# Kernel tuning notes

Measured on AMD Instinct MI355X. Metric: run time of the kernel, lower is better.

Reference implementation:

```python
import jax, jax.numpy as jnp
import numpy as np
import math

S, B, H, NH, HD = 2048, 1, 4096, 32, 128
ROT = HD // 2  # 2D RoPE: each half of head_dim gets its own rotary embedding


def _rotate_half(x):
    x1, x2 = jnp.split(x, 2, axis=-1)
    return jnp.concatenate((-x2, x1), axis=-1)


def _rope_tables(max_pos, dim):
    inv_freq = 1.0 / (10000.0 ** (jnp.arange(0, dim, 2, dtype=jnp.float32) / dim))
    freqs = jnp.arange(max_pos, dtype=jnp.float32)[:, None] * inv_freq[None, :]  # [P, dim/2]
    emb = jnp.concatenate((freqs, freqs), axis=-1)  # [P, dim]
    return jnp.cos(emb), jnp.sin(emb)


def _apply_rope(q, k, cos_t, sin_t, pid):
    # q,k: [S,B,NH,ROT]; pid: [S,B]
    c = cos_t[pid][:, :, None, :]  # [S,B,1,ROT]
    s = sin_t[pid][:, :, None, :]
    return q * c + _rotate_half(q) * s, k * c + _rotate_half(k) * s


def setup_inputs() -> dict:
    key = jax.random.key(0)
    k1, k2, k3, k4, k5 = jax.random.split(key, 5)
    hidden_states = jax.random.normal(k1, (S, B, H), dtype=jnp.float32)
    pos = jnp.arange(S, dtype=jnp.int32)[None, :]          # [1,S] standard positions
    blk = jnp.zeros((1, S), dtype=jnp.int32)                # block positions (pre-gmask all zeros)
    position_ids = jnp.stack([pos, blk], axis=1)            # [B,2,S]
    # causal mask: True = masked out
    attention_mask = jnp.triu(jnp.ones((S, S), dtype=bool), k=1)[None, None]  # [B,1,S,S]
    Wqkv = jax.random.normal(k2, (3 * H, H), dtype=jnp.float32) * 0.02
    bqkv = jax.random.normal(k3, (3 * H,), dtype=jnp.float32) * 0.02
    Wd = jax.random.normal(k4, (H, H), dtype=jnp.float32) * 0.02
    bd = jax.random.normal(k5, (H,), dtype=jnp.float32) * 0.02
    return {"hidden_states": hidden_states, "position_ids": position_ids,
            "attention_mask": attention_mask, "layer_id": 5,
            "Wqkv": Wqkv, "bqkv": bqkv, "Wd": Wd, "bd": bd}


def reference(hidden_states, position_ids, attention_mask, layer_id, Wqkv, bqkv, Wd, bd):
    # QKV projection: [S,B,H] -> [S,B,NH,3*HD]
    mixed = hidden_states @ Wqkv.T + bqkv
    mixed = mixed.reshape(S, B, NH, 3 * HD)
    q, k, v = jnp.split(mixed, 3, axis=-1)  # each [S,B,NH,HD]

    # 2D rotary position embedding on the two head-dim halves
    q1, q2 = jnp.split(q, 2, axis=-1)
    k1, k2 = jnp.split(k, 2, axis=-1)
    cos_t, sin_t = _rope_tables(S, ROT)
    pid = position_ids[:, 0, :].T   # [S,B]
    bid = position_ids[:, 1, :].T   # [S,B]
    q1, k1 = _apply_rope(q1, k1, cos_t, sin_t, pid)
    q2, k2 = _apply_rope(q2, k2, cos_t, sin_t, bid)
    q = jnp.concatenate([q1, q2], axis=-1)
    k = jnp.concatenate([k1, k2], axis=-1)

    # layer-scaled attention scores
    coeff = float(layer_id + 1)
    q = q / (math.sqrt(HD) * coeff)
    scores = jnp.einsum('sbnd,tbnd->bnst', q, k)  # [B,NH,S,S]
    scores = jnp.where(attention_mask, jnp.float32(-10000.0), scores)
    scores = scores.astype(jnp.float32) * coeff
    probs = jax.nn.softmax(scores, axis=-1).astype(hidden_states.dtype)

    ctx = jnp.einsum('bnst,tbnd->sbnd', probs, v).reshape(S, B, NH * HD)
    return ctx @ Wd.T + bd  # [S,B,H]
```

## Files before the change

kernel.cpp:

```cpp
#include <hip/hip_runtime.h>


#define S_LEN 2048
#define NHEAD 32
#define HDIM 128
#define HID 4096

typedef float f32x4 __attribute__((ext_vector_type(4)));
typedef __bf16 bf16x8 __attribute__((ext_vector_type(8)));
typedef __bf16 bf16x4 __attribute__((ext_vector_type(4)));
typedef _Float16 f16x4 __attribute__((ext_vector_type(4)));
typedef _Float16 f16x8 __attribute__((ext_vector_type(8)));

__device__ __forceinline__ void gload16(const void* g, void* l) {
  __builtin_amdgcn_global_load_lds(
      (const __attribute__((address_space(1))) void*)g,
      (__attribute__((address_space(3))) void*)l, 16, 0, 0);
}

__global__ __launch_bounds__(256) void cvt_f32_bf16_kernel(
    const float* __restrict__ in, __bf16* __restrict__ out, int n4) {
  int i = blockIdx.x * 256 + threadIdx.x;
  if (i >= n4) return;
  f32x4 v = *(const f32x4*)(in + (size_t)i * 4);
  bf16x4 o;
  o[0] = (__bf16)v[0]; o[1] = (__bf16)v[1];
  o[2] = (__bf16)v[2]; o[3] = (__bf16)v[3];
  *(bf16x4*)(out + (size_t)i * 4) = o;
}

__device__ __forceinline__ void stage_half(const __bf16* __restrict__ G,
                                           int grow0, int Kstride, int kofs,
                                           __bf16* lds_half, int tid) {
#pragma unroll
  for (int i = 0; i < 2; ++i) {
    int idx = i * 512 + tid;
    int rr = idx >> 3;
    int offp = (idx & 7) * 16;
    int off = offp ^ ((rr & 7) << 4);
    const char* src =
        (const char*)(G + (size_t)(grow0 + rr) * Kstride + kofs) + off;
    char* dst = (char*)lds_half + idx * 16;
    gload16(src, dst);
  }
}

__device__ __forceinline__ bf16x8 ldsfrag(const __bf16* hb, int rowin, int ks,
                                          int lg) {
  int off = ((ks * 64 + lg * 16) ^ ((rowin & 7) << 4));
  return *(const bf16x8*)((const char*)hb + rowin * 128 + off);
}

#define READ_A(DST, SLOT)                                                     \
  _Pragma("unroll") for (int mi = 0; mi < 4; ++mi)                            \
      _Pragma("unroll") for (int ks = 0; ks < 2; ++ks) DST[mi][ks] =          \
      ldsfrag(SLOT, wm * 64 + mi * 16 + lr, ks, lg);

#define READ_B(DST, SLOT)                                                     \
  _Pragma("unroll") for (int nj = 0; nj < 2; ++nj)                            \
      _Pragma("unroll") for (int ks = 0; ks < 2; ++ks) DST[nj][ks] =          \
      ldsfrag(SLOT, wn * 32 + nj * 16 + lr, ks, lg);

#define MFMA_Q(MH, NH, AFR, BFR)                                              \
  __builtin_amdgcn_s_setprio(1);                                              \
  _Pragma("unroll") for (int mi = 0; mi < 4; ++mi)                            \
      _Pragma("unroll") for (int nj = 0; nj < 2; ++nj)                        \
          _Pragma("unroll") for (int ks = 0; ks < 2; ++ks)                    \
              acc[MH][NH][mi][nj] =                                           \
      __builtin_amdgcn_mfma_f32_16x16x32_bf16(AFR[mi][ks], BFR[nj][ks],       \
                                              acc[MH][NH][mi][nj], 0, 0, 0);  \
  __builtin_amdgcn_s_setprio(0);

#define BAR asm volatile("s_barrier" ::: "memory");

template <int OUT_MODE>
__global__ __launch_bounds__(512, 2) void gemm256_kernel(
    const __bf16* __restrict__ A, const __bf16* __restrict__ B,
    const float* __restrict__ bias, void* __restrict__ Cout, int M, int N,
    int Kstride, int klen, int mtiles, int ksplit) {
  __shared__ __align__(16) __bf16 As[2][2][128 * 64];
  __shared__ __align__(16) __bf16 Bs[2][2][128 * 64];
  const int tid = threadIdx.x;
  int bid = blockIdx.x;
  int kh = 0;
  if (ksplit == 2) { kh = bid & 1; bid >>= 1; }
  const int kbase = kh * klen;
  int per_patch = mtiles * 8;
  int p = bid / per_patch, r = bid % per_patch;
  int mt = r % mtiles, nt = p * 8 + r / mtiles;
  int m0 = mt * 256, n0 = nt * 256;
  const int wid = tid >> 6, l = tid & 63;
  const int wm = wid >> 2, wn = wid & 3;
  const int lr = l & 15, lg = l >> 4;
  const int nk = klen >> 6;

  f32x4 acc[2][2][4][2];
#pragma unroll
  for (int a = 0; a < 2; ++a)
#pragma unroll
    for (int b = 0; b < 2; ++b)
#pragma unroll
      for (int c = 0; c < 4; ++c)
#pragma unroll
        for (int d = 0; d < 2; ++d) acc[a][b][c][d] = 0.f;

  stage_half(A, m0, Kstride, kbase, &As[0][0][0], tid);
  stage_half(B, n0, Kstride, kbase, &Bs[0][0][0], tid);
  stage_half(B, n0 + 128, Kstride, kbase, &Bs[0][1][0], tid);
  stage_half(A, m0 + 128, Kstride, kbase, &As[0][1][0], tid);
  if (nk > 1) {
    stage_half(A, m0, Kstride, kbase + 64, &As[1][0][0], tid);
    stage_half(B, n0, Kstride, kbase + 64, &Bs[1][0][0], tid);
    stage_half(B, n0 + 128, Kstride, kbase + 64, &Bs[1][1][0], tid);
    asm volatile("s_waitcnt vmcnt(6)" ::: "memory");
  } else {
    asm volatile("s_waitcnt vmcnt(0)" ::: "memory");
  }
  BAR;

  for (int t = 0; t < nk; ++t) {
    const int cur = t & 1, nxt = cur ^ 1;
    const int kt1 = kbase + (t + 1) * 64;
    const int kt2 = kbase + (t + 2) * 64;
    const bool s1 = (t + 1 < nk), s2 = (t + 2 < nk);
    bf16x8 a[4][2], b0[2][2], b1[2][2];

    READ_A(a, &As[cur][0][0]);
    READ_B(b0, &Bs[cur][0][0]);
    if (s1) stage_half(A, m0 + 128, Kstride, kt1, &As[nxt][1][0], tid);
    BAR;
    MFMA_Q(0, 0, a, b0);

    READ_B(b1, &Bs[cur][1][0]);
    if (s2) stage_half(A, m0, Kstride, kt2, &As[cur][0][0], tid);
    BAR;
    MFMA_Q(0, 1, a, b1);

    READ_A(a, &As[cur][1][0]);
    if (s2) stage_half(B, n0 + 128, Kstride, kt2, &Bs[cur][1][0], tid);
    BAR;
    MFMA_Q(1, 1, a, b1);

    if (s2) stage_half(B, n0, Kstride, kt2, &Bs[cur][0][0], tid);
    BAR;
    MFMA_Q(1, 0, a, b0);
    if (s2)
      asm volatile("s_waitcnt vmcnt(6)" ::: "memory");
    else
      asm volatile("s_waitcnt vmcnt(0)" ::: "memory");
  }

  float* outF = (float*)Cout;
  if (OUT_MODE == 2) outF += (size_t)kh * M * N;
#pragma unroll
  for (int mh = 0; mh < 2; ++mh)
#pragma unroll
    for (int nh = 0; nh < 2; ++nh)
#pragma unroll
      for (int mi = 0; mi < 4; ++mi)
#pragma unroll
        for (int nj = 0; nj < 2; ++nj) {
          int row = m0 + mh * 128 + wm * 64 + mi * 16 + lg * 4;
          int col = n0 + nh * 128 + wn * 32 + nj * 16 + lr;
          float bv = (OUT_MODE == 2) ? 0.f : bias[col];
          f32x4 v = acc[mh][nh][mi][nj];
#pragma unroll
          for (int j = 0; j < 4; ++j) {
            float o = v[j] + bv;
            if (OUT_MODE == 1)
              ((__bf16*)Cout)[(size_t)(row + j) * N + col] = (__bf16)o;
            else
              outF[(size_t)(row + j) * N + col] = o;
          }
        }
}

__global__ __launch_bounds__(256) void reduce_addbias_kernel(
    const float* __restrict__ p0, const float* __restrict__ p1,
    const float* __restrict__ bias, float* __restrict__ out) {
  int i = blockIdx.x * 256 + threadIdx.x;
  int col = (i * 4) & (HID - 1);
  f32x4 a = *(const f32x4*)(p0 + (size_t)i * 4);
  f32x4 b = *(const f32x4*)(p1 + (size_t)i * 4);
  f32x4 c = *(const f32x4*)(bias + col);
  a = a + b + c;
  *(f32x4*)(out + (size_t)i * 4) = a;
}

__global__ __launch_bounds__(256) void rope_kernel(
    const __bf16* __restrict__ qkv, const int* __restrict__ pos_ids,
    __bf16* __restrict__ Q, __bf16* __restrict__ K, _Float16* __restrict__ VT) {
  int h = blockIdx.x & 31, sb = blockIdx.x >> 5;
  int s0 = sb * 64;
  int t = threadIdx.x;
  __shared__ float cs[64][2][2][32];
  __shared__ _Float16 vs[64][132];

  for (int idx = t; idx < 64 * 64; idx += 256) {
    int sl = idx >> 6, half = (idx >> 5) & 1, i = idx & 31;
    int p = pos_ids[half * S_LEN + s0 + sl];
    float f = powf(10000.f, -(float)i / 32.f);
    float ang = (float)p * f;
    cs[sl][half][0][i] = cosf(ang);
    cs[sl][half][1][i] = sinf(ang);
  }
#pragma unroll
  for (int c = 0; c < 4; c++) {
    int chunk = c * 256 + t;
    int slv = chunk >> 4, co = (chunk & 15) * 8;
    const __bf16* vsrc =
        qkv + (size_t)(s0 + slv) * (NHEAD * 3 * HDIM) + h * 384 + 256 + co;
    bf16x8 vv = *(const bf16x8*)vsrc;
    f16x4 a, b;
#pragma unroll
    for (int j = 0; j < 4; j++) {
      a[j] = (_Float16)(float)vv[j];
      b[j] = (_Float16)(float)vv[4 + j];
    }
    *(f16x4*)&vs[slv][co] = a;
    *(f16x4*)&vs[slv][co + 4] = b;
  }
  __syncthreads();

  {
    int sl = t >> 2, role = t & 3;
    int isK = role >> 1, half = role & 1;
    const __bf16* src = qkv + (size_t)(s0 + sl) * (NHEAD * 3 * HDIM) + h * 384 +
                        isK * 128 + half * 64;
    float scale = isK ? 1.f : 0.08838834764831845f;
    float x[64];
    bf16x8 buf[8];
#pragma unroll
    for (int c = 0; c < 8; c++) buf[c] = *(const bf16x8*)(src + c * 8);
#pragma unroll
    for (int c = 0; c < 8; c++)
#pragma unroll
      for (int j = 0; j < 8; j++) x[c * 8 + j] = (float)buf[c][j];
    bf16x8 ob[8];
#pragma unroll
    for (int i = 0; i < 64; i++) {
      int ii = i & 31;
      float cv = cs[sl][half][0][ii], sv = cs[sl][half][1][ii];
      float partner = (i < 32) ? x[i + 32] : x[i - 32];
      float sgn = (i < 32) ? -1.f : 1.f;
      float o = (x[i] * cv + sgn * partner * sv) * scale;
      ob[i >> 3][i & 7] = (__bf16)o;
    }
    __bf16* dst = (isK ? K : Q) + ((size_t)h * S_LEN + s0 + sl) * HDIM + half * 64;
#pragma unroll
    for (int c = 0; c < 8; c++) *(bf16x8*)(dst + c * 8) = ob[c];
  }

#pragma unroll
  for (int c = 0; c < 4; c++) {
    int chunk = c * 256 + t;
    int d = chunk >> 3, so = (chunk & 7) * 8;
    f16x8 o;
#pragma unroll
    for (int j = 0; j < 8; j++) o[j] = vs[so + j][d];
    *(f16x8*)(VT + ((size_t)h * HDIM + d) * S_LEN + s0 + so) = o;
  }
}

__global__ __launch_bounds__(256, 2) void attn_kernel(
    const __bf16* __restrict__ Q, const __bf16* __restrict__ K,
    const _Float16* __restrict__ VT, __bf16* __restrict__ ctx) {
  int b = blockIdx.x;
  int h = b & 31;
  int x = b >> 5;
  int qb = (b < 256) ? (15 - x) : (x - 8);
  int w = threadIdx.x >> 6, l = threadIdx.x & 63;
  int lr = l & 15, lg = l >> 4;
  int q0 = qb * 128 + w * 32;
  const __bf16* Qh = Q + (size_t)h * S_LEN * HDIM;
  const __bf16* Kh = K + (size_t)h * S_LEN * HDIM;
  const _Float16* Vh = VT + (size_t)h * HDIM * S_LEN;

  bf16x8 qfA[4], qfB[4];
#pragma unroll
  for (int kk = 0; kk < 4; kk++) {
    qfA[kk] = *(const bf16x8*)(Qh + (size_t)(q0 + lr) * HDIM + kk * 32 + lg * 8);
    qfB[kk] =
        *(const bf16x8*)(Qh + (size_t)(q0 + 16 + lr) * HDIM + kk * 32 + lg * 8);
  }

  f32x4 accA[8], accB[8];
#pragma unroll
  for (int tt = 0; tt < 8; tt++) { accA[tt] = 0.f; accB[tt] = 0.f; }
  float mA = -INFINITY, lsA = 0.f, mB = -INFINITY, lsB = 0.f;
  int qgA = q0 + lr, qgB = q0 + 16 + lr;
  int qmax = q0 + 31;

  for (int kv0 = 0; kv0 <= qmax; kv0 += 32) {
    f32x4 stA0 = 0.f, stA1 = 0.f, stB0 = 0.f, stB1 = 0.f;
#pragma unroll
    for (int kk = 0; kk < 4; kk++) {
      bf16x8 kf0 =
          *(const bf16x8*)(Kh + (size_t)(kv0 + lr) * HDIM + kk * 32 + lg * 8);
      bf16x8 kf1 = *(const bf16x8*)(Kh + (size_t)(kv0 + 16 + lr) * HDIM +
                                    kk * 32 + lg * 8);
      stA0 = __builtin_amdgcn_mfma_f32_16x16x32_bf16(kf0, qfA[kk], stA0, 0, 0, 0);
      stB0 = __builtin_amdgcn_mfma_f32_16x16x32_bf16(kf0, qfB[kk], stB0, 0, 0, 0);
      stA1 = __builtin_amdgcn_mfma_f32_16x16x32_bf16(kf1, qfA[kk], stA1, 0, 0, 0);
      stB1 = __builtin_amdgcn_mfma_f32_16x16x32_bf16(kf1, qfB[kk], stB1, 0, 0, 0);
    }

    f16x4 vb0[8], vb1[8];
#pragma unroll
    for (int tt = 0; tt < 8; tt++) {
      const _Float16* vcol = Vh + (size_t)(tt * 16 + lr) * S_LEN;
      vb0[tt] = *(const f16x4*)(vcol + kv0 + lg * 4);
      vb1[tt] = *(const f16x4*)(vcol + kv0 + 16 + lg * 4);
    }

    float tmA = -INFINITY, tmB = -INFINITY;
#pragma unroll
    for (int j = 0; j < 4; j++) {
      int kvg0 = kv0 + lg * 4 + j;
      int kvg1 = kvg0 + 16;
      if (kvg0 > qgA) stA0[j] = -INFINITY;
      if (kvg1 > qgA) stA1[j] = -INFINITY;
      if (kvg0 > qgB) stB0[j] = -INFINITY;
      if (kvg1 > qgB) stB1[j] = -INFINITY;
      tmA = fmaxf(tmA, fmaxf(stA0[j], stA1[j]));
      tmB = fmaxf(tmB, fmaxf(stB0[j], stB1[j]));
    }
    tmA = fmaxf(tmA, __shfl_xor(tmA, 16));
    tmA = fmaxf(tmA, __shfl_xor(tmA, 32));
    tmB = fmaxf(tmB, __shfl_xor(tmB, 16));
    tmB = fmaxf(tmB, __shfl_xor(tmB, 32));
    int need = __any((tmA > mA) || (tmB > mB));
    float mnA = fmaxf(mA, tmA), mnB = fmaxf(mB, tmB);

    f16x4 paA0, paA1, paB0, paB1;
    float tsA = 0.f, tsB = 0.f;
#pragma unroll
    for (int j = 0; j < 4; j++) {
      float pA0 = __expf(stA0[j] - mnA);
      float pA1 = __expf(stA1[j] - mnA);
      float pB0 = __expf(stB0[j] - mnB);
      float pB1 = __expf(stB1[j] - mnB);
      tsA += pA0 + pA1;
      tsB += pB0 + pB1;
      paA0[j] = (_Float16)pA0; paA1[j] = (_Float16)pA1;
      paB0[j] = (_Float16)pB0; paB1[j] = (_Float16)pB1;
    }
    tsA += __shfl_xor(tsA, 16);
    tsA += __shfl_xor(tsA, 32);
    tsB += __shfl_xor(tsB, 16);
    tsB += __shfl_xor(tsB, 32);

    if (need) {
      float scA = __expf(mA - mnA), scB = __expf(mB - mnB);
      lsA = lsA * scA + tsA;
      lsB = lsB * scB + tsB;
      float sAj[4], sBj[4];
#pragma unroll
      for (int j = 0; j < 4; j++) {
        sAj[j] = __shfl(scA, lg * 4 + j);
        sBj[j] = __shfl(scB, lg * 4 + j);
      }
#pragma unroll
      for (int tt = 0; tt < 8; tt++)
#pragma unroll
        for (int j = 0; j < 4; j++) {
          accA[tt][j] *= sAj[j];
          accB[tt][j] *= sBj[j];
        }
    } else {
      lsA += tsA;
      lsB += tsB;
    }
    mA = mnA; mB = mnB;

#pragma unroll
    for (int tt = 0; tt < 8; tt++) {
      accA[tt] =
          __builtin_amdgcn_mfma_f32_16x16x16f16(paA0, vb0[tt], accA[tt], 0, 0, 0);
      accB[tt] =
          __builtin_amdgcn_mfma_f32_16x16x16f16(paB0, vb0[tt], accB[tt], 0, 0, 0);
      accA[tt] =
          __builtin_amdgcn_mfma_f32_16x16x16f16(paA1, vb1[tt], accA[tt], 0, 0, 0);
      accB[tt] =
          __builtin_amdgcn_mfma_f32_16x16x16f16(paB1, vb1[tt], accB[tt], 0, 0, 0);
    }
  }

  float rA[4], rB[4];
#pragma unroll
  for (int j = 0; j < 4; j++) {
    rA[j] = 1.f / __shfl(lsA, lg * 4 + j);
    rB[j] = 1.f / __shfl(lsB, lg * 4 + j);
  }
#pragma unroll
  for (int tt = 0; tt < 8; tt++) {
#pragma unroll
    for (int j = 0; j < 4; j++) {
      int qoA = q0 + lg * 4 + j;
      int qoB = q0 + 16 + lg * 4 + j;
      ctx[(size_t)qoA * (NHEAD * HDIM) + h * HDIM + tt * 16 + lr] =
          (__bf16)(accA[tt][j] * rA[j]);
      ctx[(size_t)qoB * (NHEAD * HDIM) + h * HDIM + tt * 16 + lr] =
          (__bf16)(accB[tt][j] * rB[j]);
    }
  }
}

extern "C" void kernel_launch(void* const* d_in, const int* in_sizes, int n_in,
                              void* d_out, int out_size, void* d_ws,
                              size_t ws_size, hipStream_t stream) {
  const float* hs = (const float*)d_in[0];
  const int* pos_ids = (const int*)d_in[1];
  const float* Wqkv = (const float*)d_in[4];
  const float* bqkv = (const float*)d_in[5];
  const float* Wd = (const float*)d_in[6];
  const float* bd = (const float*)d_in[7];
  float* out = (float*)d_out;

  char* ws = (char*)d_ws;
  constexpr size_t OFF_W = 16777216ULL;
  constexpr size_t OFF_QKV = OFF_W + 100663296ULL;
  constexpr size_t OFF_Q = OFF_QKV + 50331648ULL;
  constexpr size_t OFF_K = OFF_Q + 16777216ULL;
  constexpr size_t OFF_V = OFF_K + 16777216ULL;
  __bf16* hsb = (__bf16*)(ws);
  __bf16* wqkvb = (__bf16*)(ws + OFF_W);
  __bf16* wdb = (__bf16*)(ws + OFF_W);
  float* pk = (float*)(ws + OFF_W + 33554432ULL);
  __bf16* qkvb = (__bf16*)(ws + OFF_QKV);
  __bf16* ctxb = qkvb;
  __bf16* Qb = (__bf16*)(ws + OFF_Q);
  __bf16* Kb = (__bf16*)(ws + OFF_K);
  _Float16* Vtb = (_Float16*)(ws + OFF_V);

  cvt_f32_bf16_kernel<<<(S_LEN * HID) / 4 / 256, 256, 0, stream>>>(
      hs, hsb, S_LEN * HID / 4);
  cvt_f32_bf16_kernel<<<(3 * HID * HID) / 4 / 256, 256, 0, stream>>>(
      Wqkv, wqkvb, 3 * HID * HID / 4);

  gemm256_kernel<1><<<8 * 48, 512, 0, stream>>>(hsb, wqkvb, bqkv, qkvb, S_LEN,
                                                3 * HID, HID, HID, 8, 1);

  cvt_f32_bf16_kernel<<<(HID * HID) / 4 / 256, 256, 0, stream>>>(
      Wd, wdb, HID * HID / 4);

  rope_kernel<<<NHEAD * (S_LEN / 64), 256, 0, stream>>>(qkvb, pos_ids, Qb, Kb,
                                                        Vtb);

  attn_kernel<<<NHEAD * (S_LEN / 128), 256, 0, stream>>>(Qb, Kb, Vtb, ctxb);

  gemm256_kernel<2><<<2 * 8 * 16, 512, 0, stream>>>(ctxb, wdb, bd, pk, S_LEN,
                                                    HID, HID, HID / 2, 8, 2);
  reduce_addbias_kernel<<<(S_LEN * HID) / 4 / 256, 256, 0, stream>>>(
      pk, pk + (size_t)S_LEN * HID, bd, out);
}
```

Before: 565.7 us.

## Switch GEMMs to 128x256 tiles and drop split-K reduction for output projection

Replaces the 256x256-tile GEMM with a 128x256-tile kernel in which each wave computes a 64x64 sub-tile and the pipeline runs two k-substeps per 64-wide stage. The QKV projection now launches twice as many blocks, and the output projection drops split-K plus the separate reduce/bias kernel, writing fp32 output with bias directly. The aim is better CU occupancy and wave balance, and removing the partial-sum round trip through memory. In exchange each block has lower arithmetic intensity per loaded byte, and the output GEMM has only 256 blocks.

```diff
diff --git a/kernel.cpp b/kernel.cpp
--- a/kernel.cpp
+++ b/kernel.cpp
@@ -51,140 +51,110 @@
   return *(const bf16x8*)((const char*)hb + rowin * 128 + off);
 }
 
-#define READ_A(DST, SLOT)                                                     \
-  _Pragma("unroll") for (int mi = 0; mi < 4; ++mi)                            \
-      _Pragma("unroll") for (int ks = 0; ks < 2; ++ks) DST[mi][ks] =          \
-      ldsfrag(SLOT, wm * 64 + mi * 16 + lr, ks, lg);
-
-#define READ_B(DST, SLOT)                                                     \
-  _Pragma("unroll") for (int nj = 0; nj < 2; ++nj)                            \
-      _Pragma("unroll") for (int ks = 0; ks < 2; ++ks) DST[nj][ks] =          \
-      ldsfrag(SLOT, wn * 32 + nj * 16 + lr, ks, lg);
-
-#define MFMA_Q(MH, NH, AFR, BFR)                                              \
-  __builtin_amdgcn_s_setprio(1);                                              \
-  _Pragma("unroll") for (int mi = 0; mi < 4; ++mi)                            \
-      _Pragma("unroll") for (int nj = 0; nj < 2; ++nj)                        \
-          _Pragma("unroll") for (int ks = 0; ks < 2; ++ks)                    \
-              acc[MH][NH][mi][nj] =                                           \
-      __builtin_amdgcn_mfma_f32_16x16x32_bf16(AFR[mi][ks], BFR[nj][ks],       \
-                                              acc[MH][NH][mi][nj], 0, 0, 0);  \
-  __builtin_amdgcn_s_setprio(0);
-
 #define BAR asm volatile("s_barrier" ::: "memory");
 
-template <int OUT_MODE>
-__global__ __launch_bounds__(512, 2) void gemm256_kernel(
+template <int OUT_BF16>
+__global__ __launch_bounds__(512, 2) void gemm128_kernel(
     const __bf16* __restrict__ A, const __bf16* __restrict__ B,
     const float* __restrict__ bias, void* __restrict__ Cout, int M, int N,
-    int Kstride, int klen, int mtiles, int ksplit) {
-  __shared__ __align__(16) __bf16 As[2][2][128 * 64];
+    int K, int mtiles) {
+  __shared__ __align__(16) __bf16 As[2][128 * 64];
   __shared__ __align__(16) __bf16 Bs[2][2][128 * 64];
   const int tid = threadIdx.x;
   int bid = blockIdx.x;
-  int kh = 0;
-  if (ksplit == 2) { kh = bid & 1; bid >>= 1; }
-  const int kbase = kh * klen;
   int per_patch = mtiles * 8;
   int p = bid / per_patch, r = bid % per_patch;
   int mt = r % mtiles, nt = p * 8 + r / mtiles;
-  int m0 = mt * 256, n0 = nt * 256;
+  int m0 = mt * 128, n0 = nt * 256;
   const int wid = tid >> 6, l = tid & 63;
   const int wm = wid >> 2, wn = wid & 3;
   const int lr = l & 15, lg = l >> 4;
-  const int nk = klen >> 6;
-
-  f32x4 acc[2][2][4][2];
-#pragma unroll
-  for (int a = 0; a < 2; ++a)
-#pragma unroll
-    for (int b = 0; b < 2; ++b)
-#pragma unroll
-      for (int c = 0; c < 4; ++c)
-#pragma unroll
-        for (int d = 0; d < 2; ++d) acc[a][b][c][d] = 0.f;
-
-  stage_half(A, m0, Kstride, kbase, &As[0][0][0], tid);
-  stage_half(B, n0, Kstride, kbase, &Bs[0][0][0], tid);
-  stage_half(B, n0 + 128, Kstride, kbase, &Bs[0][1][0], tid);
-  stage_half(A, m0 + 128, Kstride, kbase, &As[0][1][0], tid);
-  if (nk > 1) {
-    stage_half(A, m0, Kstride, kbase + 64, &As[1][0][0], tid);
-    stage_half(B, n0, Kstride, kbase + 64, &Bs[1][0][0], tid);
-    stage_half(B, n0 + 128, Kstride, kbase + 64, &Bs[1][1][0], tid);
-    asm volatile("s_waitcnt vmcnt(6)" ::: "memory");
-  } else {
-    asm volatile("s_waitcnt vmcnt(0)" ::: "memory");
-  }
+  const int nk = K >> 6;
+
+  f32x4 acc[4][4];
+#pragma unroll
+  for (int a = 0; a < 4; ++a)
+#pragma unroll
+    for (int b = 0; b < 4; ++b) acc[a][b] = 0.f;
+
+  const int bhalf = wn >> 1;
+  const int br0 = (wn & 1) * 64;
+
+  stage_half(A, m0, K, 0, &As[0][0], tid);
+  stage_half(B, n0, K, 0, &Bs[0][0][0], tid);
+  stage_half(B, n0 + 128, K, 0, &Bs[0][1][0], tid);
+  stage_half(A, m0, K, 64, &As[1][0], tid);
+  stage_half(B, n0, K, 64, &Bs[1][0][0], tid);
+  stage_half(B, n0 + 128, K, 64, &Bs[1][1][0], tid);
+  asm volatile("s_waitcnt vmcnt(6)" ::: "memory");
   BAR;
 
   for (int t = 0; t < nk; ++t) {
-    const int cur = t & 1, nxt = cur ^ 1;
-    const int kt1 = kbase + (t + 1) * 64;
-    const int kt2 = kbase + (t + 2) * 64;
-    const bool s1 = (t + 1 < nk), s2 = (t + 2 < nk);
-    bf16x8 a[4][2], b0[2][2], b1[2][2];
-
-    READ_A(a, &As[cur][0][0]);
-    READ_B(b0, &Bs[cur][0][0]);
-    if (s1) stage_half(A, m0 + 128, Kstride, kt1, &As[nxt][1][0], tid);
+    const int cur = t & 1;
+    const int kt2 = (t + 2) * 64;
+    const bool s2 = (t + 2 < nk);
+    const __bf16* bslot = &Bs[cur][bhalf][0];
+    bf16x8 a0[4], b0[4], a1[4], b1[4];
+
+#pragma unroll
+    for (int mi = 0; mi < 4; ++mi)
+      a0[mi] = ldsfrag(&As[cur][0], wm * 64 + mi * 16 + lr, 0, lg);
+#pragma unroll
+    for (int nj = 0; nj < 4; ++nj)
+      b0[nj] = ldsfrag(bslot, br0 + nj * 16 + lr, 0, lg);
     BAR;
-    MFMA_Q(0, 0, a, b0);
-
-    READ_B(b1, &Bs[cur][1][0]);
-    if (s2) stage_half(A, m0, Kstride, kt2, &As[cur][0][0], tid);
+    __builtin_amdgcn_s_setprio(1);
+#pragma unroll
+    for (int mi = 0; mi < 4; ++mi)
+#pragma unroll
+      for (int nj = 0; nj < 4; ++nj)
+        acc[mi][nj] = __builtin_amdgcn_mfma_f32_16x16x32_bf16(
+            a0[mi], b0[nj], acc[mi][nj], 0, 0, 0);
+    __builtin_amdgcn_s_setprio(0);
+
+#pragma unroll
+    for (int mi = 0; mi < 4; ++mi)
+      a1[mi] = ldsfrag(&As[cur][0], wm * 64 + mi * 16 + lr, 1, lg);
+#pragma unroll
+    for (int nj = 0; nj < 4; ++nj)
+      b1[nj] = ldsfrag(bslot, br0 + nj * 16 + lr, 1, lg);
     BAR;
-    MFMA_Q(0, 1, a, b1);
-
-    READ_A(a, &As[cur][1][0]);
-    if (s2) stage_half(B, n0 + 128, Kstride, kt2, &Bs[cur][1][0], tid);
-    BAR;
-    MFMA_Q(1, 1, a, b1);
-
-    if (s2) stage_half(B, n0, Kstride, kt2, &Bs[cur][0][0], tid);
-    BAR;
-    MFMA_Q(1, 0, a, b0);
+    if (s2) {
+      stage_half(A, m0, K, kt2, &As[cur][0], tid);
+      stage_half(B, n0, K, kt2, &Bs[cur][0][0], tid);
+      stage_half(B, n0 + 128, K, kt2, &Bs[cur][1][0], tid);
+    }
+    __builtin_amdgcn_s_setprio(1);
+#pragma unroll
+    for (int mi = 0; mi < 4; ++mi)
+#pragma unroll
+      for (int nj = 0; nj < 4; ++nj)
+        acc[mi][nj] = __builtin_amdgcn_mfma_f32_16x16x32_bf16(
+            a1[mi], b1[nj], acc[mi][nj], 0, 0, 0);
+    __builtin_amdgcn_s_setprio(0);
     if (s2)
       asm volatile("s_waitcnt vmcnt(6)" ::: "memory");
     else
       asm volatile("s_waitcnt vmcnt(0)" ::: "memory");
   }
 
-  float* outF = (float*)Cout;
-  if (OUT_MODE == 2) outF += (size_t)kh * M * N;
-#pragma unroll
-  for (int mh = 0; mh < 2; ++mh)
-#pragma unroll
-    for (int nh = 0; nh < 2; ++nh)
-#pragma unroll
-      for (int mi = 0; mi < 4; ++mi)
-#pragma unroll
-        for (int nj = 0; nj < 2; ++nj) {
-          int row = m0 + mh * 128 + wm * 64 + mi * 16 + lg * 4;
-          int col = n0 + nh * 128 + wn * 32 + nj * 16 + lr;
-          float bv = (OUT_MODE == 2) ? 0.f : bias[col];
-          f32x4 v = acc[mh][nh][mi][nj];
-#pragma unroll
-          for (int j = 0; j < 4; ++j) {
-            float o = v[j] + bv;
-            if (OUT_MODE == 1)
-              ((__bf16*)Cout)[(size_t)(row + j) * N + col] = (__bf16)o;
-            else
-              outF[(size_t)(row + j) * N + col] = o;
-          }
-        }
-}
-
-__global__ __launch_bounds__(256) void reduce_addbias_kernel(
-    const float* __restrict__ p0, const float* __restrict__ p1,
-    const float* __restrict__ bias, float* __restrict__ out) {
-  int i = blockIdx.x * 256 + threadIdx.x;
-  int col = (i * 4) & (HID - 1);
-  f32x4 a = *(const f32x4*)(p0 + (size_t)i * 4);
-  f32x4 b = *(const f32x4*)(p1 + (size_t)i * 4);
-  f32x4 c = *(const f32x4*)(bias + col);
-  a = a + b + c;
-  *(f32x4*)(out + (size_t)i * 4) = a;
+#pragma unroll
+  for (int mi = 0; mi < 4; ++mi)
+#pragma unroll
+    for (int nj = 0; nj < 4; ++nj) {
+      int row = m0 + wm * 64 + mi * 16 + lg * 4;
+      int col = n0 + wn * 64 + nj * 16 + lr;
+      float bv = bias[col];
+      f32x4 v = acc[mi][nj];
+#pragma unroll
+      for (int j = 0; j < 4; ++j) {
+        float o = v[j] + bv;
+        if (OUT_BF16)
+          ((__bf16*)Cout)[(size_t)(row + j) * N + col] = (__bf16)o;
+        else
+          ((float*)Cout)[(size_t)(row + j) * N + col] = o;
+      }
+    }
 }
 
 __global__ __launch_bounds__(256) void rope_kernel(
@@ -426,7 +396,6 @@
   __bf16* hsb = (__bf16*)(ws);
   __bf16* wqkvb = (__bf16*)(ws + OFF_W);
   __bf16* wdb = (__bf16*)(ws + OFF_W);
-  float* pk = (float*)(ws + OFF_W + 33554432ULL);
   __bf16* qkvb = (__bf16*)(ws + OFF_QKV);
   __bf16* ctxb = qkvb;
   __bf16* Qb = (__bf16*)(ws + OFF_Q);
@@ -438,8 +407,8 @@
   cvt_f32_bf16_kernel<<<(3 * HID * HID) / 4 / 256, 256, 0, stream>>>(
       Wqkv, wqkvb, 3 * HID * HID / 4);
 
-  gemm256_kernel<1><<<8 * 48, 512, 0, stream>>>(hsb, wqkvb, bqkv, qkvb, S_LEN,
-                                                3 * HID, HID, HID, 8, 1);
+  gemm128_kernel<1><<<16 * 48, 512, 0, stream>>>(hsb, wqkvb, bqkv, qkvb,
+                                                 S_LEN, 3 * HID, HID, 16);
 
   cvt_f32_bf16_kernel<<<(HID * HID) / 4 / 256, 256, 0, stream>>>(
       Wd, wdb, HID * HID / 4);
@@ -449,8 +418,6 @@
 
   attn_kernel<<<NHEAD * (S_LEN / 128), 256, 0, stream>>>(Qb, Kb, Vtb, ctxb);
 
-  gemm256_kernel<2><<<2 * 8 * 16, 512, 0, stream>>>(ctxb, wdb, bd, pk, S_LEN,
-                                                    HID, HID, HID / 2, 8, 2);
-  reduce_addbias_kernel<<<(S_LEN * HID) / 4 / 256, 256, 0, stream>>>(
-      pk, pk + (size_t)S_LEN * HID, bd, out);
-}
+  gemm128_kernel<0><<<16 * 16, 512, 0, stream>>>(ctxb, wdb, bd, out, S_LEN,
+                                                 HID, HID, 16);
+}
```

Result: slower. 611.2 us (+8.0%).
